# Kernel tuning notes

Hardware: AMD Instinct MI355X
Metric: run time of the kernel (lower is better)

The kernel has to match this reference:

```python
import jax, jax.numpy as jnp
import numpy as np

B, C, H, W = 32, 128, 32, 32
E, K, D, HID = 16, 2, 128, 512  # nbExperts, topK, nbIn=nbOut, hidden=4*max(nbIn,nbOut)


def setup_inputs() -> dict:
    key = jax.random.key(0)
    ks = jax.random.split(key, 6)
    init = lambda k, shape, fan: (jax.random.normal(k, shape, jnp.float32) / np.sqrt(fan)).astype(jnp.float32)
    return {
        "x": jax.random.normal(ks[0], (B, C, H, W), jnp.float32),
        "gate_w": init(ks[1], (D, E), D),
        "gate_b": jnp.zeros((E,), jnp.float32),
        "noise_w": init(ks[2], (D, E), D),
        "noise_b": jnp.zeros((E,), jnp.float32),
        "w1": init(ks[3], (E, D, HID), D),
        "b1": jnp.zeros((E, HID), jnp.float32),
        "w2": init(ks[4], (E, HID, D), HID),
        "b2": jnp.zeros((E, D), jnp.float32),
        "top_k": K,
    }


def reference(x, gate_w, gate_b, noise_w, noise_b, w1, b1, w2, b2, top_k):
    b, c, h, w = x.shape
    xt = x.transpose(0, 2, 3, 1).reshape(-1, c)  # [T, D] tokens (fromCNN path)
    T = xt.shape[0]

    # --- GatingWithNoise: gate(x) + randn * softplus(noise(x)) ---
    logits = xt @ gate_w + gate_b                      # [T, E]
    noise_sd = jax.nn.softplus(xt @ noise_w + noise_b)  # [T, E]
    noise = jax.random.normal(jax.random.key(42), logits.shape, logits.dtype)
    logits = logits + noise * noise_sd

    # --- top-k, softmax over k, scatter to dense [T, E] gate matrix ---
    top_vals, top_idx = jax.lax.top_k(logits, top_k)   # [T, K]
    probs = jax.nn.softmax(top_vals, axis=1)           # [T, K]
    gates = jnp.zeros((T, E), x.dtype).at[jnp.arange(T)[:, None], top_idx].set(probs)

    # --- dense path: run every expert, weighted combine ---
    hdn = jax.nn.relu(jnp.einsum('td,edh->teh', xt, w1) + b1)  # [T, E, HID]
    eo = jnp.einsum('teh,ehd->ted', hdn, w2) + b2              # [T, E, D]
    out = jnp.einsum('te,ted->td', gates, eo)                  # [T, D]

    out = out.reshape(b, h, w, c).transpose(0, 3, 1, 2)        # back to NCHW
    gates = gates.reshape(b, h, w, E)
    return out, gates
```

## Files before the change

kernel.cpp:

```cpp
#include <hip/hip_runtime.h>
#include <stdint.h>

#define NB       32
#define NC       128
#define NHW      1024
#define NT       32768
#define NE       16
#define NHID     512
#define NGBLK    512

typedef __attribute__((ext_vector_type(8))) short short8v;
typedef __attribute__((ext_vector_type(4))) float f32x4;
typedef __attribute__((ext_vector_type(2))) uint32_t uint2v;

__device__ __forceinline__ unsigned short f2bf(float f) {
    uint32_t u = __float_as_uint(f);
    uint32_t r = u + 0x7fffu + ((u >> 16) & 1u);
    return (unsigned short)(r >> 16);
}
__device__ __forceinline__ float bf2f(unsigned short u) {
    return __uint_as_float(((uint32_t)u) << 16);
}

__device__ __forceinline__ void gll16(const void* g, void* l) {
    __builtin_amdgcn_global_load_lds(
        (const __attribute__((address_space(1))) uint32_t*)g,
        (__attribute__((address_space(3))) uint32_t*)l, 16, 0, 0);
}

#define WAIT_VM0_LGKM0() asm volatile("s_waitcnt vmcnt(0) lgkmcnt(0)" ::: "memory")
#define WAIT_LGKM()      asm volatile("s_waitcnt lgkmcnt(0)" ::: "memory")
#define SBAR()           { asm volatile("" ::: "memory"); __builtin_amdgcn_s_barrier(); asm volatile("" ::: "memory"); }

__device__ __forceinline__ uint32_t rotl32(uint32_t x, uint32_t d) {
    return (x << d) | (x >> (32u - d));
}

__device__ __forceinline__ void threefry2x32_20(uint32_t k0, uint32_t k1,
                                                uint32_t& x0, uint32_t& x1) {
    const uint32_t ks0 = k0, ks1 = k1, ks2 = k0 ^ k1 ^ 0x1BD11BDAu;
    x0 += ks0; x1 += ks1;
#define TFR(r) { x0 += x1; x1 = rotl32(x1, r); x1 ^= x0; }
    TFR(13u) TFR(15u) TFR(26u) TFR(6u)
    x0 += ks1; x1 += ks2 + 1u;
    TFR(17u) TFR(29u) TFR(16u) TFR(24u)
    x0 += ks2; x1 += ks0 + 2u;
    TFR(13u) TFR(15u) TFR(26u) TFR(6u)
    x0 += ks0; x1 += ks1 + 3u;
    TFR(17u) TFR(29u) TFR(16u) TFR(24u)
    x0 += ks1; x1 += ks2 + 4u;
    TFR(13u) TFR(15u) TFR(26u) TFR(6u)
    x0 += ks2; x1 += ks0 + 5u;
#undef TFR
}

__device__ __forceinline__ float erfinv_xla_f32(float x) {
    float w = -log1pf(-x * x);
    float p;
    if (w < 5.0f) {
        w = w - 2.5f;
        p = 2.81022636e-08f;
        p = fmaf(p, w, 3.43273939e-07f);
        p = fmaf(p, w, -3.5233877e-06f);
        p = fmaf(p, w, -4.39150654e-06f);
        p = fmaf(p, w, 0.00021858087f);
        p = fmaf(p, w, -0.00125372503f);
        p = fmaf(p, w, -0.00417768164f);
        p = fmaf(p, w, 0.246640727f);
        p = fmaf(p, w, 1.50140941f);
    } else {
        w = sqrtf(w) - 3.0f;
        p = -0.000200214257f;
        p = fmaf(p, w, 0.000100950558f);
        p = fmaf(p, w, 0.00134934322f);
        p = fmaf(p, w, -0.00367342844f);
        p = fmaf(p, w, 0.00573950773f);
        p = fmaf(p, w, -0.0076224613f);
        p = fmaf(p, w, 0.00943887047f);
        p = fmaf(p, w, 1.00167406f);
        p = fmaf(p, w, 2.83297682f);
    }
    return p * x;
}

__device__ __forceinline__ float jax_noise_elem(uint32_t i) {
    uint32_t x0 = 0u, x1 = i;
    threefry2x32_20(0u, 42u, x0, x1);
    uint32_t bits = x0 ^ x1;
    float f = __uint_as_float(0x3f800000u | (bits >> 9)) - 1.0f;
    const float lo = -0.99999994f;
    float u = f * 2.0f + lo;
    u = fmaxf(lo, u);
    return 1.41421354f * erfinv_xla_f32(u);
}

__global__ __launch_bounds__(256) void moe_gate_tw_kernel(
    const float* __restrict__ x,
    const float* __restrict__ gate_w, const float* __restrict__ gate_b,
    const float* __restrict__ noise_w, const float* __restrict__ noise_b,
    float* __restrict__ gates_out,
    int*   __restrict__ top_idx,
    float* __restrict__ top_prob,
    int*   __restrict__ rank,
    int*   __restrict__ bcnt,
    unsigned short* __restrict__ xtb,
    const float* __restrict__ w1, unsigned short* __restrict__ w1bt,
    const float* __restrict__ w2, unsigned short* __restrict__ w2bt,
    int do_new)
{
    __shared__ union { float lw[32 * 160]; float ts[64][65]; } sm;
    __shared__ int lcnt[16];

    const int tid = threadIdx.x;

    if (blockIdx.x >= NGBLK) {
        int blk = blockIdx.x - NGBLK;
        const float* src;  unsigned short* dst;  int R, C;
        if (blk < 256) { src = w1; dst = w1bt; R = 128; C = 512; }
        else           { src = w2; dst = w2bt; R = 512; C = 128; blk -= 256; }
        const int nr = R >> 6, ncc = C >> 6;
        const int e = blk / (nr * ncc);
        const int rem = blk % (nr * ncc);
        const int rt = rem / ncc, ct = rem % ncc;
        const float* S = src + (size_t)e * R * C + (size_t)(rt * 64) * C + ct * 64;
        unsigned short* D = dst + (size_t)e * R * C + (size_t)(ct * 64) * R + rt * 64;
        #pragma unroll
        for (int i = 0; i < 16; ++i) {
            int lin = i * 256 + tid;
            int r = lin >> 6, c = lin & 63;
            sm.ts[r][c] = S[(size_t)r * C + c];
        }
        __syncthreads();
        #pragma unroll
        for (int i = 0; i < 16; ++i) {
            int lin = i * 256 + tid;
            int c = lin >> 6, r = lin & 63;
            D[(size_t)c * R + r] = f2bf(sm.ts[r][c]);
        }
        return;
    }

    const int tl  = tid >> 2;
    const int q   = tid & 3;
    const int t   = blockIdx.x * 64 + tl;
    const int b   = t >> 10, hw = t & 1023;

    if (tid < 16) lcnt[tid] = 0;

    for (int idx = tid; idx < 4096; idx += 256) {
        int ci = idx >> 7;
        int r  = idx & 127;
        int qq = r >> 5, e = r & 31;
        int c  = qq * 32 + ci;
        float v = (e < 16) ? gate_w[c * 16 + e] : noise_w[c * 16 + (e - 16)];
        sm.lw[ci * 160 + qq * 40 + e] = v;
    }
    __syncthreads();

    float acc[32];
    #pragma unroll
    for (int e = 0; e < 32; ++e) acc[e] = 0.f;

    unsigned short xh[32];
    const float* xq = x + (size_t)b * (NC * NHW) + (size_t)(q * 32) * NHW + hw;
    const float* wq = sm.lw + q * 40;
    #pragma unroll 4
    for (int ci = 0; ci < 32; ++ci) {
        float xv = xq[(size_t)ci << 10];
        xh[ci] = f2bf(xv);
        const f32x4* wr = (const f32x4*)(wq + ci * 160);
        #pragma unroll
        for (int j = 0; j < 8; ++j) {
            f32x4 w4 = wr[j];
            #pragma unroll
            for (int k = 0; k < 4; ++k)
                acc[j * 4 + k] = fmaf(xv, w4[k], acc[j * 4 + k]);
        }
    }

    if (do_new) {
        #pragma unroll
        for (int j = 0; j < 4; ++j) {
            short8v v;
            #pragma unroll
            for (int k = 0; k < 8; ++k) v[k] = (short)xh[j * 8 + k];
            *(short8v*)(xtb + (size_t)t * 128 + q * 32 + j * 8) = v;
        }
    }

    #pragma unroll
    for (int e = 0; e < 32; ++e) {
        acc[e] += __shfl_xor(acc[e], 1);
        acc[e] += __shfl_xor(acc[e], 2);
    }

    float lg[4];
    #pragma unroll
    for (int j = 0; j < 4; ++j) {
        int e = q * 4 + j;
        float g  = acc[e] + gate_b[e];
        float an = acc[16 + e] + noise_b[e];
        float sd = fmaxf(an, 0.f) + log1pf(expf(-fabsf(an)));
        float nz = jax_noise_elem((uint32_t)t * 16u + (uint32_t)e);
        lg[j] = fmaf(nz, sd, g);
    }

    float v1 = lg[0], v2 = -INFINITY;
    int   i1 = q * 4, i2 = 0x7fffffff;
    #pragma unroll
    for (int j = 1; j < 4; ++j) {
        float v = lg[j]; int e = q * 4 + j;
        if (v > v1) { v2 = v1; i2 = i1; v1 = v; i1 = e; }
        else if (v > v2) { v2 = v; i2 = e; }
    }
    #pragma unroll
    for (int m = 1; m <= 2; m <<= 1) {
        float pv1 = __shfl_xor(v1, m), pv2 = __shfl_xor(v2, m);
        int   pi1 = __shfl_xor(i1, m), pi2 = __shfl_xor(i2, m);
        bool pBest = (pv1 > v1) || (pv1 == v1 && pi1 < i1);
        float c2v; int c2i;
        if (pBest) { c2v = v1;  c2i = i1;  v1 = pv1; i1 = pi1;
                     if (!((c2v > pv2) || (c2v == pv2 && c2i < pi2))) { c2v = pv2; c2i = pi2; }
        } else     { c2v = pv1; c2i = pi1;
                     if (!((c2v > v2)  || (c2v == v2  && c2i < i2)))  { c2v = v2;  c2i = i2;  }
        }
        v2 = c2v; i2 = c2i;
    }

    float qq = expf(v2 - v1);
    float s  = 1.0f + qq;
    float p1 = 1.0f / s;
    float p2 = qq / s;

    f32x4 g4;
    #pragma unroll
    for (int j = 0; j < 4; ++j) {
        int e = q * 4 + j;
        g4[j] = (e == i1) ? p1 : ((e == i2) ? p2 : 0.f);
    }
    *(f32x4*)(gates_out + (size_t)t * 16 + q * 4) = g4;

    if (q == 0) {
        top_idx[t * 2 + 0] = i1;  top_idx[t * 2 + 1] = i2;
        top_prob[t * 2 + 0] = p1; top_prob[t * 2 + 1] = p2;
        if (do_new) {
            int r1 = atomicAdd(&lcnt[i1], 1);
            int r2 = atomicAdd(&lcnt[i2], 1);
            rank[t * 2 + 0] = r1;
            rank[t * 2 + 1] = r2;
        }
    }
    if (do_new) {
        __syncthreads();
        if (tid < 16) bcnt[blockIdx.x * 16 + tid] = lcnt[tid];
    }
}

__global__ __launch_bounds__(256) void scatter2_kernel(
    const int* __restrict__ bcnt,
    const int* __restrict__ top_idx, const int* __restrict__ rank,
    int* __restrict__ poff, int* __restrict__ blk2e,
    int* __restrict__ blk2chunk, int* __restrict__ total_chunks,
    int* __restrict__ pair_tok, int* __restrict__ slot_of)
{
    __shared__ int ps[16][17];
    __shared__ int cum[16][17];
    __shared__ int scnt[16];
    __shared__ int snch[16];
    __shared__ int scum[17];
    __shared__ int spoff[16];
    __shared__ int lbase[2][16];

    const int tid = threadIdx.x;
    const int e = tid >> 4, s = tid & 15;

    int a = 0;
    for (int b = s * 32; b < s * 32 + 32; ++b)
        a += bcnt[b * 16 + e];
    ps[e][s] = a;
    __syncthreads();

    if (tid < 16) {
        int run = 0;
        for (int ss = 0; ss < 16; ++ss) { cum[tid][ss] = run; run += ps[tid][ss]; }
        scnt[tid] = run;
        snch[tid] = (run + 255) >> 8;
    }
    __syncthreads();

    if (tid == 0) {
        int cc = 0, off = 0;
        for (int ee = 0; ee < 16; ++ee) {
            scum[ee] = cc; spoff[ee] = off;
            cc += snch[ee]; off += snch[ee] << 8;
        }
        scum[16] = cc;
    }
    __syncthreads();

    if (tid < 32) {
        int ee = tid >> 1, w = tid & 1;
        int g = (int)blockIdx.x * 2 + w;
        int sg = g >> 5;
        int part = cum[ee][sg];
        for (int b = sg * 32; b < g; ++b) part += bcnt[b * 16 + ee];
        lbase[w][ee] = spoff[ee] + part;
    }

    if (blockIdx.x == 0) {
        if (tid < 16) poff[tid] = spoff[tid];
        if (tid == 0) *total_chunks = scum[16];
        const int tot = scum[16];
        for (int idx = tid; idx < tot; idx += 256) {
            int ee = 0;
            #pragma unroll
            for (int k = 0; k < 15; ++k)
                if (idx >= scum[k + 1]) ee = k + 1;
            blk2e[idx] = ee;
            blk2chunk[idx] = idx - scum[ee];
        }
        for (int ee = 0; ee < 16; ++ee) {
            int start = spoff[ee] + scnt[ee];
            int end   = spoff[ee] + (snch[ee] << 8);
            for (int i = start + tid; i < end; i += 256)
                pair_tok[i] = -1;
        }
    }
    __syncthreads();

    int i = (int)blockIdx.x * 256 + tid;
    int t = i >> 1;
    int ee = top_idx[i];
    int g = (t >> 6) & 1;
    int slot = lbase[g][ee] + rank[i];
    pair_tok[slot] = t;
    slot_of[i] = slot;
}

__device__ __forceinline__ void stage_w1(const unsigned short* w1e, short* W1s,
                                         int hcn, int wid, int lane) {
    #pragma unroll
    for (int k2 = 0; k2 < 2; ++k2) {
        int i2 = wid * 2 + k2;
        int r2 = i2 * 4 + (lane >> 4);
        int s2 = lane & 15;
        gll16(w1e + (size_t)(hcn + r2) * 128 + ((s2 ^ (r2 & 15)) * 8),
              W1s + i2 * 512);
    }
}
__device__ __forceinline__ void stage_w2(const unsigned short* w2e, short* W2s,
                                         int hcn, int wid, int lane) {
    #pragma unroll
    for (int k2 = 0; k2 < 2; ++k2) {
        int i2 = wid * 2 + k2;
        int r2 = i2 * 8 + (lane >> 3);
        int s2 = lane & 7;
        gll16(w2e + (size_t)r2 * 512 + hcn + ((s2 ^ (r2 & 7)) * 8),
              W2s + i2 * 512);
    }
}

__global__ __launch_bounds__(512, 2) void moe_mfma_kernel(
    const unsigned short* __restrict__ xtb,
    const int* __restrict__ pair_tok, const int* __restrict__ blk2e,
    const int* __restrict__ blk2chunk, const int* __restrict__ poff,
    const int* __restrict__ total_chunks,
    const unsigned short* __restrict__ w1bt,
    const float* __restrict__ b1,
    const unsigned short* __restrict__ w2bt,
    const float* __restrict__ b2,
    unsigned short* __restrict__ pair_y)
{
    __shared__ short Hs[256 * 64];
    __shared__ short W1s[64 * 128];
    __shared__ short W2s[128 * 64];

    const int blk = (blockIdx.x & 7) * 34 + (blockIdx.x >> 3);
    if (blk >= *total_chunks) return;
    const int e  = blk2e[blk];
    const int p0 = poff[e] + (blk2chunk[blk] << 8);
    const int tid  = threadIdx.x;
    const int lane = tid & 63;
    const int wid  = tid >> 6;
    const int l16  = lane & 15;
    const int lg   = lane >> 4;

    const unsigned short* w1e = w1bt + (size_t)e * 512 * 128;
    const unsigned short* w2e = w2bt + (size_t)e * 128 * 512;

    stage_w1(w1e, W1s, 0, wid, lane);
    stage_w2(w2e, W2s, 0, wid, lane);

    short8v xa[2][4];
    #pragma unroll
    for (int ni = 0; ni < 2; ++ni) {
        int row = wid * 32 + ni * 16 + l16;
        int tok = pair_tok[p0 + row];
        #pragma unroll
        for (int kk = 0; kk < 4; ++kk) {
            short8v v = {};
            if (tok >= 0)
                v = *(const short8v*)(xtb + (size_t)tok * 128 + kk * 32 + lg * 8);
            xa[ni][kk] = v;
        }
    }

    f32x4 yacc[2][8];
    #pragma unroll
    for (int ni = 0; ni < 2; ++ni)
        #pragma unroll
        for (int nj = 0; nj < 8; ++nj)
            yacc[ni][nj] = (f32x4){0.f, 0.f, 0.f, 0.f};

    const int rowA0 = wid * 32 + l16, rowA1 = rowA0 + 16;

    for (int c = 0; c < 8; ++c) {
        WAIT_VM0_LGKM0(); SBAR();

        f32x4 hacc[4][2];
        #pragma unroll
        for (int mi = 0; mi < 4; ++mi)
            #pragma unroll
            for (int ni = 0; ni < 2; ++ni)
                hacc[mi][ni] = (f32x4){0.f, 0.f, 0.f, 0.f};

        __builtin_amdgcn_s_setprio(1);
        #pragma unroll
        for (int kk = 0; kk < 4; ++kk) {
            int slot = kk * 4 + lg;
            #pragma unroll
            for (int mi = 0; mi < 4; ++mi) {
                int hr = mi * 16 + l16;
                short8v wfr = *(const short8v*)(W1s + hr * 128 + ((slot ^ (hr & 15)) * 8));
                #pragma unroll
                for (int ni = 0; ni < 2; ++ni)
                    hacc[mi][ni] = __builtin_amdgcn_mfma_f32_16x16x32_bf16(
                        wfr, xa[ni][kk], hacc[mi][ni], 0, 0, 0);
            }
        }
        __builtin_amdgcn_s_setprio(0);

        #pragma unroll
        for (int mi = 0; mi < 4; ++mi) {
            int h0 = mi * 16 + lg * 4;
            f32x4 b1v = *(const f32x4*)(b1 + e * 512 + (c << 6) + h0);
            #pragma unroll
            for (int ni = 0; ni < 2; ++ni) {
                int tok = wid * 32 + ni * 16 + l16;
                float v0 = fmaxf(hacc[mi][ni][0] + b1v[0], 0.f);
                float v1 = fmaxf(hacc[mi][ni][1] + b1v[1], 0.f);
                float v2 = fmaxf(hacc[mi][ni][2] + b1v[2], 0.f);
                float v3 = fmaxf(hacc[mi][ni][3] + b1v[3], 0.f);
                uint32_t lo = (uint32_t)f2bf(v0) | ((uint32_t)f2bf(v1) << 16);
                uint32_t hi = (uint32_t)f2bf(v2) | ((uint32_t)f2bf(v3) << 16);
                int slot = h0 >> 3;
                int addr = tok * 64 + ((slot ^ (tok & 7)) << 3) + (h0 & 7);
                *(uint2v*)(Hs + addr) = (uint2v){lo, hi};
            }
        }
        WAIT_LGKM(); SBAR();

        if (c < 7) stage_w1(w1e, W1s, (c + 1) << 6, wid, lane);

        __builtin_amdgcn_s_setprio(1);
        #pragma unroll
        for (int kk = 0; kk < 2; ++kk) {
            int slot = kk * 4 + lg;
            short8v a0 = *(const short8v*)(Hs + rowA0 * 64 + ((slot ^ (rowA0 & 7)) * 8));
            short8v a1 = *(const short8v*)(Hs + rowA1 * 64 + ((slot ^ (rowA1 & 7)) * 8));
            #pragma unroll
            for (int nj = 0; nj < 8; ++nj) {
                int dr = nj * 16 + l16;
                short8v bfr = *(const short8v*)(W2s + dr * 64 + ((slot ^ (dr & 7)) * 8));
                yacc[0][nj] = __builtin_amdgcn_mfma_f32_16x16x32_bf16(a0, bfr, yacc[0][nj], 0, 0, 0);
                yacc[1][nj] = __builtin_amdgcn_mfma_f32_16x16x32_bf16(a1, bfr, yacc[1][nj], 0, 0, 0);
            }
        }
        __builtin_amdgcn_s_setprio(0);
        WAIT_LGKM(); SBAR();

        if (c < 7) stage_w2(w2e, W2s, (c + 1) << 6, wid, lane);
    }

    #pragma unroll
    for (int nj = 0; nj < 8; ++nj) {
        int d = nj * 16 + l16;
        float b2v = b2[e * 128 + d];
        #pragma unroll
        for (int ni = 0; ni < 2; ++ni) {
            #pragma unroll
            for (int r = 0; r < 4; ++r) {
                int m = wid * 32 + ni * 16 + lg * 4 + r;
                pair_y[(size_t)(p0 + m) * 128 + d] = f2bf(yacc[ni][nj][r] + b2v);
            }
        }
    }
}

__global__ __launch_bounds__(256) void combine_kernel(
    const unsigned short* __restrict__ pair_y, const int* __restrict__ slot_of,
    const float* __restrict__ top_prob, float* __restrict__ out)
{
    __shared__ float ob[64][129];
    const int blk = blockIdx.x;
    const int b = blk >> 4;
    const int hw0 = (blk & 15) << 6;
    const int tid = threadIdx.x;
    #pragma unroll
    for (int i = 0; i < 4; ++i) {
        int lin = i * 256 + tid;
        int tl = lin >> 4, dg = lin & 15;
        int t = b * 1024 + hw0 + tl;
        int s0 = slot_of[t * 2], s1 = slot_of[t * 2 + 1];
        float p0 = top_prob[t * 2], p1 = top_prob[t * 2 + 1];
        short8v y0 = *(const short8v*)(pair_y + (size_t)s0 * 128 + dg * 8);
        short8v y1 = *(const short8v*)(pair_y + (size_t)s1 * 128 + dg * 8);
        #pragma unroll
        for (int j = 0; j < 8; ++j)
            ob[tl][dg * 8 + j] = p0 * bf2f((unsigned short)y0[j]) + p1 * bf2f((unsigned short)y1[j]);
    }
    __syncthreads();
    #pragma unroll
    for (int i = 0; i < 32; ++i) {
        int lin = i * 256 + tid;
        int d = lin >> 6, hwl = lin & 63;
        out[((size_t)b * 128 + d) * 1024 + hw0 + hwl] = ob[hwl][d];
    }
}

__global__ __launch_bounds__(256) void moe_expert_kernel(
    const float* __restrict__ x,
    const int* __restrict__ top_idx, const float* __restrict__ top_prob,
    const float* __restrict__ w1, const float* __restrict__ b1,
    const float* __restrict__ w2, const float* __restrict__ b2,
    float* __restrict__ out)
{
    __shared__ float xsB[128];
    __shared__ float hb[512];

    const int tid = threadIdx.x;
    const int t = blockIdx.x;
    const int b = t >> 10, hw = t & 1023;

    if (tid < 128)
        xsB[tid] = x[((size_t)b * 128 + tid) * NHW + hw];
    __syncthreads();

    float oacc = 0.f;
    #pragma unroll
    for (int k = 0; k < 2; ++k) {
        const int e = top_idx[t * 2 + k];
        const float pw = top_prob[t * 2 + k];
        const float* W1 = w1 + (size_t)e * (128 * 512);
        float a0 = 0.f, a1 = 0.f;
        for (int d = 0; d < 128; ++d) {
            float xv = xsB[d];
            a0 = fmaf(xv, W1[d * 512 + tid], a0);
            a1 = fmaf(xv, W1[d * 512 + tid + 256], a1);
        }
        hb[tid]       = fmaxf(a0 + b1[e * 512 + tid], 0.f);
        hb[tid + 256] = fmaxf(a1 + b1[e * 512 + tid + 256], 0.f);
        __syncthreads();
        if (tid < 128) {
            const float* W2 = w2 + (size_t)e * (512 * 128);
            float a = 0.f;
            for (int h = 0; h < 512; ++h)
                a = fmaf(hb[h], W2[h * 128 + tid], a);
            oacc = fmaf(pw, a + b2[e * 128 + tid], oacc);
        }
        __syncthreads();
    }
    if (tid < 128)
        out[((size_t)b * 128 + tid) * NHW + hw] = oacc;
}

extern "C" void kernel_launch(void* const* d_in, const int* in_sizes, int n_in,
                              void* d_out, int out_size, void* d_ws, size_t ws_size,
                              hipStream_t stream) {
    const float* x       = (const float*)d_in[0];
    const float* gate_w  = (const float*)d_in[1];
    const float* gate_b  = (const float*)d_in[2];
    const float* noise_w = (const float*)d_in[3];
    const float* noise_b = (const float*)d_in[4];
    const float* w1      = (const float*)d_in[5];
    const float* b1      = (const float*)d_in[6];
    const float* w2      = (const float*)d_in[7];
    const float* b2      = (const float*)d_in[8];

    float* out   = (float*)d_out;
    float* gates = out + (size_t)NB * NC * NHW;

    const size_t OFF_POFF   = 0;
    const size_t OFF_TOTAL  = 1024;
    const size_t OFF_B2E    = 4096;
    const size_t OFF_B2C    = 8192;
    const size_t OFF_TIDX   = 12288;
    const size_t OFF_RANK   = OFF_TIDX  + (size_t)NT * 2 * 4;
    const size_t OFF_SLOT   = OFF_RANK  + (size_t)NT * 2 * 4;
    const size_t OFF_PROB   = OFF_SLOT  + (size_t)NT * 2 * 4;
    const size_t OFF_BCNT   = OFF_PROB  + (size_t)NT * 2 * 4;
    const size_t OFF_XTB    = OFF_BCNT  + (size_t)NGBLK * 16 * 4;
    const size_t OFF_W1BT   = OFF_XTB   + (size_t)NT * 128 * 2;
    const size_t OFF_W2BT   = OFF_W1BT  + (size_t)NE * 512 * 128 * 2;
    const size_t OFF_PTOK   = OFF_W2BT  + (size_t)NE * 128 * 512 * 2;
    const size_t NPAIR_PAD  = 69632;
    const size_t OFF_PAIRY  = OFF_PTOK  + NPAIR_PAD * 4;
    const size_t NEED       = OFF_PAIRY + NPAIR_PAD * 128 * 2;

    char* ws = (char*)d_ws;
    int*   poff     = (int*)(ws + OFF_POFF);
    int*   total_ch = (int*)(ws + OFF_TOTAL);
    int*   blk2e    = (int*)(ws + OFF_B2E);
    int*   blk2c    = (int*)(ws + OFF_B2C);
    int*   top_idx  = (int*)(ws + OFF_TIDX);
    int*   rank     = (int*)(ws + OFF_RANK);
    int*   slot_of  = (int*)(ws + OFF_SLOT);
    float* top_prob = (float*)(ws + OFF_PROB);
    int*   bcnt     = (int*)(ws + OFF_BCNT);
    unsigned short* xtb    = (unsigned short*)(ws + OFF_XTB);
    unsigned short* w1bt   = (unsigned short*)(ws + OFF_W1BT);
    unsigned short* w2bt   = (unsigned short*)(ws + OFF_W2BT);
    int*   pair_tok = (int*)(ws + OFF_PTOK);
    unsigned short* pair_y = (unsigned short*)(ws + OFF_PAIRY);

    const int use_new = (ws_size >= NEED) ? 1 : 0;

    moe_gate_tw_kernel<<<use_new ? (NGBLK + 512) : NGBLK, 256, 0, stream>>>(
        x, gate_w, gate_b, noise_w, noise_b,
        gates, top_idx, top_prob, rank, bcnt, xtb,
        w1, w1bt, w2, w2bt, use_new);

    if (use_new) {
        scatter2_kernel<<<256, 256, 0, stream>>>(bcnt, top_idx, rank,
                                                 poff, blk2e, blk2c, total_ch,
                                                 pair_tok, slot_of);
        moe_mfma_kernel<<<272, 512, 0, stream>>>(
            xtb, pair_tok, blk2e, blk2c, poff, total_ch,
            w1bt, b1, w2bt, b2, pair_y);
        combine_kernel<<<512, 256, 0, stream>>>(pair_y, slot_of, top_prob, out);
    } else {
        moe_expert_kernel<<<NT, 256, 0, stream>>>(
            x, top_idx, top_prob, w1, b1, w2, b2, out);
    }
}
```

Measured before the change: 102.1 us.

## Double-buffer expert weights, pass hidden activations via shuffles, drop Hs LDS

Replaces the LDS round-trip for hidden activations with register packing and cross-lane shuffles that build the second GEMM's A fragments directly. W1/W2 tiles are double-buffered so the next chunk's loads are issued right after the first barrier, which removes two barriers per chunk. X rows are re-read from global memory inside the loop instead of being held in registers, and launch bounds now target 4 blocks per CU. The aim is more overlap and occupancy, at the cost of extra global reloads, shuffle work and register pressure that could cause spills.

Result: slower. 136.2 us (+33.4%).

```diff
diff --git a/kernel.cpp b/kernel.cpp
--- a/kernel.cpp
+++ b/kernel.cpp
@@ -11,7 +11,6 @@
 
 typedef __attribute__((ext_vector_type(8))) short short8v;
 typedef __attribute__((ext_vector_type(4))) float f32x4;
-typedef __attribute__((ext_vector_type(2))) uint32_t uint2v;
 
 __device__ __forceinline__ unsigned short f2bf(float f) {
     uint32_t u = __float_as_uint(f);
@@ -29,7 +28,6 @@
 }
 
 #define WAIT_VM0_LGKM0() asm volatile("s_waitcnt vmcnt(0) lgkmcnt(0)" ::: "memory")
-#define WAIT_LGKM()      asm volatile("s_waitcnt lgkmcnt(0)" ::: "memory")
 #define SBAR()           { asm volatile("" ::: "memory"); __builtin_amdgcn_s_barrier(); asm volatile("" ::: "memory"); }
 
 __device__ __forceinline__ uint32_t rotl32(uint32_t x, uint32_t d) {
@@ -360,7 +358,7 @@
     }
 }
 
-__global__ __launch_bounds__(512, 2) void moe_mfma_kernel(
+__global__ __launch_bounds__(512, 4) void moe_mfma_kernel(
     const unsigned short* __restrict__ xtb,
     const int* __restrict__ pair_tok, const int* __restrict__ blk2e,
     const int* __restrict__ blk2chunk, const int* __restrict__ poff,
@@ -371,9 +369,8 @@
     const float* __restrict__ b2,
     unsigned short* __restrict__ pair_y)
 {
-    __shared__ short Hs[256 * 64];
-    __shared__ short W1s[64 * 128];
-    __shared__ short W2s[128 * 64];
+    __shared__ short W1s[2][64 * 128];
+    __shared__ short W2s[2][128 * 64];
 
     const int blk = (blockIdx.x & 7) * 34 + (blockIdx.x >> 3);
     if (blk >= *total_chunks) return;
@@ -388,22 +385,16 @@
     const unsigned short* w1e = w1bt + (size_t)e * 512 * 128;
     const unsigned short* w2e = w2bt + (size_t)e * 128 * 512;
 
-    stage_w1(w1e, W1s, 0, wid, lane);
-    stage_w2(w2e, W2s, 0, wid, lane);
-
-    short8v xa[2][4];
-    #pragma unroll
-    for (int ni = 0; ni < 2; ++ni) {
-        int row = wid * 32 + ni * 16 + l16;
-        int tok = pair_tok[p0 + row];
-        #pragma unroll
-        for (int kk = 0; kk < 4; ++kk) {
-            short8v v = {};
-            if (tok >= 0)
-                v = *(const short8v*)(xtb + (size_t)tok * 128 + kk * 32 + lg * 8);
-            xa[ni][kk] = v;
-        }
-    }
+    int tok0, tok1;
+    {
+        tok0 = pair_tok[p0 + wid * 32 + l16];
+        tok1 = pair_tok[p0 + wid * 32 + 16 + l16];
+    }
+    const unsigned short* xb0 = xtb + (size_t)(tok0 < 0 ? 0 : tok0) * 128;
+    const unsigned short* xb1 = xtb + (size_t)(tok1 < 0 ? 0 : tok1) * 128;
+
+    stage_w1(w1e, W1s[0], 0, wid, lane);
+    stage_w2(w2e, W2s[0], 0, wid, lane);
 
     f32x4 yacc[2][8];
     #pragma unroll
@@ -412,10 +403,20 @@
         for (int nj = 0; nj < 8; ++nj)
             yacc[ni][nj] = (f32x4){0.f, 0.f, 0.f, 0.f};
 
-    const int rowA0 = wid * 32 + l16, rowA1 = rowA0 + 16;
+    const int srcA = l16 + ((lg & 1) << 5);
+    const int srcB = srcA + 16;
+    const bool selHi = (lg & 2) != 0;
 
     for (int c = 0; c < 8; ++c) {
+        const short* W1b = W1s[c & 1];
+        const short* W2b = W2s[c & 1];
+
         WAIT_VM0_LGKM0(); SBAR();
+
+        if (c < 7) {
+            stage_w1(w1e, W1s[(c + 1) & 1], (c + 1) << 6, wid, lane);
+            stage_w2(w2e, W2s[(c + 1) & 1], (c + 1) << 6, wid, lane);
+        }
 
         f32x4 hacc[4][2];
         #pragma unroll
@@ -427,59 +428,67 @@
         __builtin_amdgcn_s_setprio(1);
         #pragma unroll
         for (int kk = 0; kk < 4; ++kk) {
+            short8v xa0 = {}, xa1 = {};
+            if (tok0 >= 0) xa0 = *(const short8v*)(xb0 + kk * 32 + lg * 8);
+            if (tok1 >= 0) xa1 = *(const short8v*)(xb1 + kk * 32 + lg * 8);
             int slot = kk * 4 + lg;
             #pragma unroll
             for (int mi = 0; mi < 4; ++mi) {
                 int hr = mi * 16 + l16;
-                short8v wfr = *(const short8v*)(W1s + hr * 128 + ((slot ^ (hr & 15)) * 8));
-                #pragma unroll
-                for (int ni = 0; ni < 2; ++ni)
-                    hacc[mi][ni] = __builtin_amdgcn_mfma_f32_16x16x32_bf16(
-                        wfr, xa[ni][kk], hacc[mi][ni], 0, 0, 0);
+                short8v wfr = *(const short8v*)(W1b + hr * 128 + ((slot ^ (hr & 15)) * 8));
+                hacc[mi][0] = __builtin_amdgcn_mfma_f32_16x16x32_bf16(wfr, xa0, hacc[mi][0], 0, 0, 0);
+                hacc[mi][1] = __builtin_amdgcn_mfma_f32_16x16x32_bf16(wfr, xa1, hacc[mi][1], 0, 0, 0);
             }
         }
         __builtin_amdgcn_s_setprio(0);
 
+        uint32_t pk[4][2][2];
         #pragma unroll
         for (int mi = 0; mi < 4; ++mi) {
             int h0 = mi * 16 + lg * 4;
             f32x4 b1v = *(const f32x4*)(b1 + e * 512 + (c << 6) + h0);
             #pragma unroll
             for (int ni = 0; ni < 2; ++ni) {
-                int tok = wid * 32 + ni * 16 + l16;
                 float v0 = fmaxf(hacc[mi][ni][0] + b1v[0], 0.f);
                 float v1 = fmaxf(hacc[mi][ni][1] + b1v[1], 0.f);
                 float v2 = fmaxf(hacc[mi][ni][2] + b1v[2], 0.f);
                 float v3 = fmaxf(hacc[mi][ni][3] + b1v[3], 0.f);
-                uint32_t lo = (uint32_t)f2bf(v0) | ((uint32_t)f2bf(v1) << 16);
-                uint32_t hi = (uint32_t)f2bf(v2) | ((uint32_t)f2bf(v3) << 16);
-                int slot = h0 >> 3;
-                int addr = tok * 64 + ((slot ^ (tok & 7)) << 3) + (h0 & 7);
-                *(uint2v*)(Hs + addr) = (uint2v){lo, hi};
+                pk[mi][ni][0] = (uint32_t)f2bf(v0) | ((uint32_t)f2bf(v1) << 16);
+                pk[mi][ni][1] = (uint32_t)f2bf(v2) | ((uint32_t)f2bf(v3) << 16);
             }
         }
-        WAIT_LGKM(); SBAR();
-
-        if (c < 7) stage_w1(w1e, W1s, (c + 1) << 6, wid, lane);
 
         __builtin_amdgcn_s_setprio(1);
         #pragma unroll
-        for (int kk = 0; kk < 2; ++kk) {
-            int slot = kk * 4 + lg;
-            short8v a0 = *(const short8v*)(Hs + rowA0 * 64 + ((slot ^ (rowA0 & 7)) * 8));
-            short8v a1 = *(const short8v*)(Hs + rowA1 * 64 + ((slot ^ (rowA1 & 7)) * 8));
+        for (int kk2 = 0; kk2 < 2; ++kk2) {
+            short8v paf[2];
+            #pragma unroll
+            for (int ni = 0; ni < 2; ++ni) {
+                uint32_t wlo0 = __shfl(pk[2 * kk2    ][ni][0], srcA);
+                uint32_t whi0 = __shfl(pk[2 * kk2 + 1][ni][0], srcA);
+                uint32_t wlo1 = __shfl(pk[2 * kk2    ][ni][1], srcA);
+                uint32_t whi1 = __shfl(pk[2 * kk2 + 1][ni][1], srcA);
+                uint32_t wlo2 = __shfl(pk[2 * kk2    ][ni][0], srcB);
+                uint32_t whi2 = __shfl(pk[2 * kk2 + 1][ni][0], srcB);
+                uint32_t wlo3 = __shfl(pk[2 * kk2    ][ni][1], srcB);
+                uint32_t whi3 = __shfl(pk[2 * kk2 + 1][ni][1], srcB);
+                union { uint32_t u[4]; short8v s; } cvt;
+                cvt.u[0] = selHi ? whi0 : wlo0;
+                cvt.u[1] = selHi ? whi1 : wlo1;
+                cvt.u[2] = selHi ? whi2 : wlo2;
+                cvt.u[3] = selHi ? whi3 : wlo3;
+                paf[ni] = cvt.s;
+            }
+            int slot = kk2 * 4 + lg;
             #pragma unroll
             for (int nj = 0; nj < 8; ++nj) {
                 int dr = nj * 16 + l16;
-                short8v bfr = *(const short8v*)(W2s + dr * 64 + ((slot ^ (dr & 7)) * 8));
-                yacc[0][nj] = __builtin_amdgcn_mfma_f32_16x16x32_bf16(a0, bfr, yacc[0][nj], 0, 0, 0);
-                yacc[1][nj] = __builtin_amdgcn_mfma_f32_16x16x32_bf16(a1, bfr, yacc[1][nj], 0, 0, 0);
+                short8v bfr = *(const short8v*)(W2b + dr * 64 + ((slot ^ (dr & 7)) * 8));
+                yacc[0][nj] = __builtin_amdgcn_mfma_f32_16x16x32_bf16(paf[0], bfr, yacc[0][nj], 0, 0, 0);
+                yacc[1][nj] = __builtin_amdgcn_mfma_f32_16x16x32_bf16(paf[1], bfr, yacc[1][nj], 0, 0, 0);
             }
         }
         __builtin_amdgcn_s_setprio(0);
-        WAIT_LGKM(); SBAR();
-
-        if (c < 7) stage_w2(w2e, W2s, (c + 1) << 6, wid, lane);
     }
 
     #pragma unroll
```
